# Kernel tuning notes

Measured on AMD Instinct MI355X. Metric: run time of the kernel, lower is better.

The kernel has to match this reference:

```python
import jax, jax.numpy as jnp
import numpy as np

B, C, CI, H, W = 4, 256, 128, 64, 64  # batch, in_channels, inter_channels, spatial


def setup_inputs() -> dict:
    key = jax.random.key(0)
    ks = jax.random.split(key, 9)
    p = lambda k, shape: jax.random.normal(k, shape, jnp.float32) * 0.05
    return {
        "x": jax.random.normal(ks[0], (B, C, H, W), jnp.float32),
        "g_w": p(ks[1], (CI, C)), "g_b": p(ks[2], (CI,)),
        "theta_w": p(ks[3], (CI, C)), "theta_b": p(ks[4], (CI,)),
        "phi_w": p(ks[5], (CI, C)), "phi_b": p(ks[6], (CI,)),
        "out_w": p(ks[7], (C, CI)), "out_b": p(ks[8], (C,)),
    }


def reference(x, g_w, g_b, theta_w, theta_b, phi_w, phi_b, out_w, out_b):
    n, c, h, w = x.shape
    xf = x.reshape(n, c, h * w)  # (b, C, N)
    # 1x1 convs as channel matmuls
    g_x = jnp.einsum('bcn,oc->bno', xf, g_w) + g_b              # (b, N, CI)
    theta_x = jnp.einsum('bcn,oc->bno', xf, theta_w) + theta_b  # (b, N, CI)
    phi_x = jnp.einsum('bcn,oc->bon', xf, phi_w) + phi_b[:, None]  # (b, CI, N)
    # 'channel' whitening: theta centered over channel axis per position,
    # phi centered over spatial axis per channel (as in source)
    theta_x = theta_x - theta_x.mean(axis=2, keepdims=True)
    phi_x = phi_x - phi_x.mean(axis=2, keepdims=True)
    # no softmax / no scaling in this forward
    pairwise = jnp.einsum('bnc,bcm->bnm', theta_x, phi_x)  # (b, N, N)
    y = jnp.einsum('bnm,bmc->bnc', pairwise, g_x)          # (b, N, CI)
    out = jnp.einsum('bnc,oc->bon', y, out_w) + out_b[:, None]  # (b, C, N)
    return x + out.reshape(n, c, h, w)
```

## Files before the change

### kernel.cpp

```cpp
#include <hip/hip_runtime.h>

constexpr int kB  = 4;
constexpr int kC  = 256;
constexpr int kCI = 128;
constexpr int kN  = 64 * 64;


constexpr int kSplits = 16;
constexpr int kSliceN = kN / kSplits;

typedef __attribute__((ext_vector_type(8))) short bf16x8;
typedef __attribute__((ext_vector_type(4))) float f32x4;

__device__ inline ushort f2b(float f) {
    unsigned u = __float_as_uint(f);
    return (ushort)((u + 0x7FFF + ((u >> 16) & 1)) >> 16);
}
__device__ inline float b2f(ushort u) { return __uint_as_float((unsigned)u << 16); }

constexpr long kOffTwcT  = 0;
constexpr long kOffTbc   = kOffTwcT + kC * kCI;
constexpr long kOffPG    = kOffTbc + kCI;
constexpr long kOffRs    = kOffPG + (long)kB * kC * kN / 2;
constexpr long kOffTpart = kOffRs + kB * kC;
constexpr long kOffT     = kOffTpart + (long)kB * kSplits * kCI * kCI;
constexpr long kOffW2t   = kOffT + kB * kCI * kCI;
constexpr long kOffMt    = kOffW2t + kB * kC * kCI;
constexpr long kOffBeta  = kOffMt + kB * kC * kC;
constexpr long kOffXT    = kOffBeta + kB * kC;

__global__ void __launch_bounds__(256, 4)
xt_kernel(const float* __restrict__ x, ushort* __restrict__ xT) {
    int b = blockIdx.z;
    int n0 = blockIdx.x * 64, c0 = blockIdx.y * 64;
    __shared__ float ft[64][66];
    int t = threadIdx.x;
    const float* xb = x + (long)b * kC * kN;
#pragma unroll
    for (int i = 0; i < 4; i++) {
        int l = t + 256 * i;
        int row = l >> 4, col4 = (l & 15) * 4;
        float4 v = *(const float4*)(xb + (long)(c0 + row) * kN + n0 + col4);
        ft[row][col4 + 0] = v.x; ft[row][col4 + 1] = v.y;
        ft[row][col4 + 2] = v.z; ft[row][col4 + 3] = v.w;
    }
    __syncthreads();
    {
        int n = t >> 2, cs = (t & 3) * 16;
        unsigned w[8];
#pragma unroll
        for (int j = 0; j < 8; j++) {
            ushort lo = f2b(ft[cs + 2 * j][n]);
            ushort hi = f2b(ft[cs + 2 * j + 1][n]);
            w[j] = (unsigned)lo | ((unsigned)hi << 16);
        }
        ushort* dst = xT + ((long)b * kN + n0 + n) * kC + c0 + cs;
        ((uint4*)dst)[0] = make_uint4(w[0], w[1], w[2], w[3]);
        ((uint4*)dst)[1] = make_uint4(w[4], w[5], w[6], w[7]);
    }
}

__global__ void centerw_kernel(const float* __restrict__ theta_w,
                               const float* __restrict__ theta_b,
                               float* __restrict__ twcT, float* __restrict__ tbc) {
    __shared__ float sm[128];
    int t = threadIdx.x;
    if (t < 128) sm[t] = theta_b[t];
    __syncthreads();
    for (int st = 64; st > 0; st >>= 1) {
        if (t < st) sm[t] += sm[t + st];
        __syncthreads();
    }
    float bmean = sm[0] * (1.f / kCI);
    float m = 0.f;
    for (int k = 0; k < kCI; k++) m += theta_w[k * kC + t];
    m *= (1.f / kCI);
    for (int k = 0; k < kCI; k++) twcT[t * kCI + k] = theta_w[k * kC + t] - m;
    if (t < 128) tbc[t] = theta_b[t] - bmean;
}

__global__ void __launch_bounds__(256, 2)
pg_mfma(const float* __restrict__ phi_w, const float* __restrict__ g_w,
        const ushort* __restrict__ xT, ushort* __restrict__ PGh) {
    int b = blockIdx.z;
    int r0 = blockIdx.y * 128, n0 = blockIdx.x * 64;
    const float* wbase = blockIdx.y == 0 ? phi_w : g_w;
    __shared__ ushort Ws[128 * 40];
    __shared__ ushort Xs[64 * 40];
    int t = threadIdx.x;
    int w = t >> 6, lane = t & 63, q = lane >> 4, ln = lane & 15;
    f32x4 acc[2][4];
#pragma unroll
    for (int i = 0; i < 2; i++)
#pragma unroll
        for (int j = 0; j < 4; j++) acc[i][j] = 0.f;
    const ushort* xTb = xT + ((long)b * kN + n0) * kC;
    for (int kc = 0; kc < kC; kc += 32) {
        __syncthreads();
#pragma unroll
        for (int it = 0; it < 4; it++) {
            int l = t + 256 * it;
            int row = l >> 3, seg = l & 7;
            float4 v = *(const float4*)(wbase + (long)row * kC + kc + seg * 4);
            ushort4 u = {f2b(v.x), f2b(v.y), f2b(v.z), f2b(v.w)};
            *(ushort4*)&Ws[row * 40 + seg * 4] = u;
        }
        {
            int row = t >> 2, seg = t & 3;
            uint4 v = *(const uint4*)(xTb + (long)row * kC + kc + seg * 8);
            *(uint4*)&Xs[row * 40 + seg * 8] = v;
        }
        __syncthreads();
        bf16x8 a[2], bb[4];
#pragma unroll
        for (int mt = 0; mt < 2; mt++)
            a[mt] = *(const bf16x8*)&Ws[(32 * w + 16 * mt + ln) * 40 + q * 8];
#pragma unroll
        for (int nt = 0; nt < 4; nt++)
            bb[nt] = *(const bf16x8*)&Xs[(16 * nt + ln) * 40 + q * 8];
#pragma unroll
        for (int mt = 0; mt < 2; mt++)
#pragma unroll
            for (int nt = 0; nt < 4; nt++)
                acc[mt][nt] = __builtin_amdgcn_mfma_f32_16x16x32_bf16(
                    a[mt], bb[nt], acc[mt][nt], 0, 0, 0);
    }
    ushort* pb = PGh + (long)b * kC * kN;
#pragma unroll
    for (int mt = 0; mt < 2; mt++)
#pragma unroll
        for (int nt = 0; nt < 4; nt++)
#pragma unroll
            for (int i = 0; i < 4; i++) {
                int row = r0 + 32 * w + 16 * mt + 4 * q + i;
                int col = n0 + 16 * nt + ln;
                pb[(long)row * kN + col] = f2b(acc[mt][nt][i]);
            }
}

__global__ void rowsum_kernel(const ushort* __restrict__ PGh, float* __restrict__ rs) {
    int br = blockIdx.x;
    const ushort* p = PGh + (long)br * kN;
    float s = 0.f;
    for (int i = threadIdx.x * 8; i < kN; i += 2048) {
        uint4 v = *(const uint4*)(p + i);
        unsigned ww[4] = {v.x, v.y, v.z, v.w};
#pragma unroll
        for (int j = 0; j < 4; j++) {
            s += __uint_as_float(ww[j] << 16);
            s += __uint_as_float(ww[j] & 0xFFFF0000u);
        }
    }
    __shared__ float sm[256];
    sm[threadIdx.x] = s;
    __syncthreads();
    for (int st = 128; st > 0; st >>= 1) {
        if (threadIdx.x < st) sm[threadIdx.x] += sm[threadIdx.x + st];
        __syncthreads();
    }
    if (threadIdx.x == 0) rs[br] = sm[0];
}

__global__ void __launch_bounds__(256, 4)
tsplit_mfma(const ushort* __restrict__ PGh, float* __restrict__ Tpart) {
    int s = blockIdx.x, b = blockIdx.z;
    int qy = blockIdx.y >> 1, qx = blockIdx.y & 1;
    long nbase = (long)s * kSliceN;
    __shared__ ushort As[64 * 40];
    __shared__ ushort Bs[64 * 40];
    int t = threadIdx.x;
    int w = t >> 6, lane = t & 63, q = lane >> 4, ln = lane & 15;
    f32x4 acc[4];
#pragma unroll
    for (int j = 0; j < 4; j++) acc[j] = 0.f;
    const ushort* Phi = PGh + ((long)b * kC + 64 * qy) * kN + nbase;
    const ushort* G2  = PGh + ((long)b * kC + kCI + 64 * qx) * kN + nbase;
    for (int kc = 0; kc < kSliceN; kc += 32) {
        __syncthreads();
        {
            int row = t >> 2, seg = t & 3;
            *(uint4*)&As[row * 40 + seg * 8] =
                *(const uint4*)(Phi + (long)row * kN + kc + seg * 8);
            *(uint4*)&Bs[row * 40 + seg * 8] =
                *(const uint4*)(G2 + (long)row * kN + kc + seg * 8);
        }
        __syncthreads();
        bf16x8 a = *(const bf16x8*)&As[(16 * w + ln) * 40 + q * 8];
#pragma unroll
        for (int nt = 0; nt < 4; nt++) {
            bf16x8 bb = *(const bf16x8*)&Bs[(16 * nt + ln) * 40 + q * 8];
            acc[nt] = __builtin_amdgcn_mfma_f32_16x16x32_bf16(a, bb, acc[nt], 0, 0, 0);
        }
    }
    float* Tp = Tpart + ((long)b * kSplits + s) * kCI * kCI;
#pragma unroll
    for (int nt = 0; nt < 4; nt++)
#pragma unroll
        for (int i = 0; i < 4; i++) {
            int c  = 64 * qy + 16 * w + 4 * q + i;
            int cp = 64 * qx + 16 * nt + ln;
            Tp[(long)c * kCI + cp] = acc[nt][i];
        }
}

__global__ void treduce_kernel(const float* __restrict__ Tpart, const float* __restrict__ rs,
                               float* __restrict__ T) {
    int idx = blockIdx.x * 256 + threadIdx.x;
    int b = idx >> 14;
    int c = (idx >> 7) & 127, cp = idx & 127;
    const float* tp = Tpart + (long)b * kSplits * kCI * kCI + (idx & 16383);
    float s = 0.f;
#pragma unroll
    for (int sl = 0; sl < kSplits; sl++) s += tp[(long)sl * kCI * kCI];
    s -= rs[b * kC + c] * rs[b * kC + kCI + cp] * (1.f / kN);
    T[idx] = s;
}

__global__ void __launch_bounds__(256, 4)
nt64_gemm(const float* __restrict__ A, const float* __restrict__ B,
          float* __restrict__ Cm, int M, int N, int K,
          long sA, long sB, long sC) {
    int b = blockIdx.z;
    const float* Ab = A + (long)b * sA;
    const float* Bb = B + (long)b * sB;
    float* Cb = Cm + (long)b * sC;
    __shared__ __align__(16) float As[16][68];
    __shared__ __align__(16) float Bs[16][68];
    int t = threadIdx.x;
    int tx = t & 15, ty = t >> 4;
    int m0 = blockIdx.y * 64, n0 = blockIdx.x * 64;
    float acc[4][4] = {};
    for (int kc = 0; kc < K; kc += 16) {
        __syncthreads();
        {
            int r = t >> 2, c4 = (t & 3) * 4;
            float4 va = *(const float4*)(Ab + (long)(m0 + r) * K + kc + c4);
            As[c4 + 0][r] = va.x; As[c4 + 1][r] = va.y;
            As[c4 + 2][r] = va.z; As[c4 + 3][r] = va.w;
            float4 vb = *(const float4*)(Bb + (long)(n0 + r) * K + kc + c4);
            Bs[c4 + 0][r] = vb.x; Bs[c4 + 1][r] = vb.y;
            Bs[c4 + 2][r] = vb.z; Bs[c4 + 3][r] = vb.w;
        }
        __syncthreads();
#pragma unroll
        for (int k = 0; k < 16; k++) {
            float4 a = *(const float4*)&As[k][4 * ty];
            float4 bv = *(const float4*)&Bs[k][4 * tx];
            float av[4] = {a.x, a.y, a.z, a.w};
            float bw[4] = {bv.x, bv.y, bv.z, bv.w};
#pragma unroll
            for (int i = 0; i < 4; i++)
#pragma unroll
                for (int j = 0; j < 4; j++) acc[i][j] += av[i] * bw[j];
        }
    }
#pragma unroll
    for (int i = 0; i < 4; i++) {
        float4 ov = {acc[i][0], acc[i][1], acc[i][2], acc[i][3]};
        *(float4*)(Cb + (long)(m0 + 4 * ty + i) * N + n0 + 4 * tx) = ov;
    }
}

__global__ void beta_kernel(const float* __restrict__ W2t, const float* __restrict__ tbc,
                            const float* __restrict__ out_b, float* __restrict__ beta) {
    int i = blockIdx.x * blockDim.x + threadIdx.x;
    if (i >= kB * kC) return;
    int o = i & (kC - 1);
    float s = out_b[o];
    const float* row = W2t + (long)i * kCI;
#pragma unroll 8
    for (int k = 0; k < kCI; k++) s += tbc[k] * row[k];
    beta[i] = s;
}

__global__ void __launch_bounds__(256, 2)
final_mfma(const float* __restrict__ x, const float* __restrict__ Mt,
           const ushort* __restrict__ xT, const float* __restrict__ beta,
           float* __restrict__ out) {
    int b = blockIdx.z;
    int o0 = blockIdx.y * 128, n0 = blockIdx.x * 64;
    const float* Mb = Mt + (long)b * kC * kC;
    __shared__ ushort Ws[128 * 40];
    __shared__ ushort Xs[64 * 40];
    int t = threadIdx.x;
    int w = t >> 6, lane = t & 63, q = lane >> 4, ln = lane & 15;
    f32x4 acc[2][4];
#pragma unroll
    for (int i = 0; i < 2; i++)
#pragma unroll
        for (int j = 0; j < 4; j++) acc[i][j] = 0.f;
    const ushort* xTb = xT + ((long)b * kN + n0) * kC;
    for (int kc = 0; kc < kC; kc += 32) {
        __syncthreads();
#pragma unroll
        for (int it = 0; it < 4; it++) {
            int l = t + 256 * it;
            int row = l >> 3, seg = l & 7;
            float4 v = *(const float4*)(Mb + (long)(o0 + row) * kC + kc + seg * 4);
            ushort4 u = {f2b(v.x), f2b(v.y), f2b(v.z), f2b(v.w)};
            *(ushort4*)&Ws[row * 40 + seg * 4] = u;
        }
        {
            int row = t >> 2, seg = t & 3;
            uint4 v = *(const uint4*)(xTb + (long)row * kC + kc + seg * 8);
            *(uint4*)&Xs[row * 40 + seg * 8] = v;
        }
        __syncthreads();
        bf16x8 a[2], bb[4];
#pragma unroll
        for (int mt = 0; mt < 2; mt++)
            a[mt] = *(const bf16x8*)&Ws[(32 * w + 16 * mt + ln) * 40 + q * 8];
#pragma unroll
        for (int nt = 0; nt < 4; nt++)
            bb[nt] = *(const bf16x8*)&Xs[(16 * nt + ln) * 40 + q * 8];
#pragma unroll
        for (int mt = 0; mt < 2; mt++)
#pragma unroll
            for (int nt = 0; nt < 4; nt++)
                acc[mt][nt] = __builtin_amdgcn_mfma_f32_16x16x32_bf16(
                    a[mt], bb[nt], acc[mt][nt], 0, 0, 0);
    }
    const float* xb = x + (long)b * kC * kN;
    float* ob = out + (long)b * kC * kN;
#pragma unroll
    for (int mt = 0; mt < 2; mt++)
#pragma unroll
        for (int nt = 0; nt < 4; nt++)
#pragma unroll
            for (int i = 0; i < 4; i++) {
                int row = o0 + 32 * w + 16 * mt + 4 * q + i;
                int col = n0 + 16 * nt + ln;
                long idx = (long)row * kN + col;
                ob[idx] = acc[mt][nt][i] + xb[idx] + beta[b * kC + row];
            }
}

extern "C" void kernel_launch(void* const* d_in, const int* in_sizes, int n_in,
                              void* d_out, int out_size, void* d_ws, size_t ws_size,
                              hipStream_t stream) {
    const float* x       = (const float*)d_in[0];
    const float* g_w     = (const float*)d_in[1];
    const float* theta_w = (const float*)d_in[3];
    const float* theta_b = (const float*)d_in[4];
    const float* phi_w   = (const float*)d_in[5];
    const float* out_w   = (const float*)d_in[7];
    const float* out_b   = (const float*)d_in[8];
    float* out = (float*)d_out;
    float* ws  = (float*)d_ws;

    float*  twcT  = ws + kOffTwcT;
    float*  tbc   = ws + kOffTbc;
    ushort* PGh   = (ushort*)(ws + kOffPG);
    float*  rs    = ws + kOffRs;
    float*  Tpart = ws + kOffTpart;
    float*  T     = ws + kOffT;
    float*  W2t   = ws + kOffW2t;
    float*  Mt    = ws + kOffMt;
    float*  beta  = ws + kOffBeta;
    ushort* xT    = (ushort*)(ws + kOffXT);

    xt_kernel<<<dim3(kN / 64, kC / 64, kB), 256, 0, stream>>>(x, xT);
    centerw_kernel<<<1, 256, 0, stream>>>(theta_w, theta_b, twcT, tbc);
    pg_mfma<<<dim3(kN / 64, 2, kB), 256, 0, stream>>>(phi_w, g_w, xT, PGh);
    rowsum_kernel<<<kB * kC, 256, 0, stream>>>(PGh, rs);
    tsplit_mfma<<<dim3(kSplits, 4, kB), 256, 0, stream>>>(PGh, Tpart);
    treduce_kernel<<<kB * kCI * kCI / 256, 256, 0, stream>>>(Tpart, rs, T);
    nt64_gemm<<<dim3(2, 4, kB), 256, 0, stream>>>(out_w, T, W2t, kC, kCI, kCI,
                                                  0, (long)kCI * kCI, (long)kC * kCI);
    nt64_gemm<<<dim3(4, 4, kB), 256, 0, stream>>>(W2t, twcT, Mt, kC, kC, kCI,
                                                  (long)kC * kCI, 0, (long)kC * kC);
    beta_kernel<<<kB, 256, 0, stream>>>(W2t, tbc, out_b, beta);
    final_mfma<<<dim3(kN / 64, 2, kB), 256, 0, stream>>>(x, Mt, xT, beta, out);
}
```

Measured before the change: 151.0 us.

## Fuse rowsum into pg_mfma, beta into Mt GEMM, parallelize centering, use bf16 residual

Row sums of the phi/g projections are now accumulated in the pg_mfma epilogue with wave shuffles and atomics, replacing the separate rowsum pass over PGh. The centering kernel is split across four blocks with a shared-memory tile, and it also zeroes the row-sum buffer. The beta bias vector is computed inside a new Mt GEMM kernel, removing the separate beta launch. The final kernel reads the residual from the bf16 transposed copy of x instead of the fp32 input, cutting that traffic at the cost of residual precision and less coalesced reads.

```diff
diff --git a/kernel.cpp b/kernel.cpp
--- a/kernel.cpp
+++ b/kernel.cpp
@@ -60,28 +60,60 @@
     }
 }
 
-__global__ void centerw_kernel(const float* __restrict__ theta_w,
-                               const float* __restrict__ theta_b,
-                               float* __restrict__ twcT, float* __restrict__ tbc) {
+__global__ void __launch_bounds__(256, 2)
+centerw_kernel(const float* __restrict__ theta_w, const float* __restrict__ theta_b,
+               float* __restrict__ twcT, float* __restrict__ tbc,
+               float* __restrict__ rs) {
+    int blk = blockIdx.x;
+    int c0 = blk * 64;
+    int t = threadIdx.x;
+    __shared__ float Ls[128][65];
+    __shared__ float part[64][4];
+    __shared__ float mean[64];
     __shared__ float sm[128];
-    int t = threadIdx.x;
-    if (t < 128) sm[t] = theta_b[t];
+    rs[blk * 256 + t] = 0.f;
+#pragma unroll
+    for (int it = 0; it < 8; it++) {
+        int l = t + 256 * it;
+        int k = l >> 4, c4 = (l & 15) * 4;
+        float4 v = *(const float4*)(theta_w + (long)k * kC + c0 + c4);
+        Ls[k][c4 + 0] = v.x; Ls[k][c4 + 1] = v.y;
+        Ls[k][c4 + 2] = v.z; Ls[k][c4 + 3] = v.w;
+    }
     __syncthreads();
-    for (int st = 64; st > 0; st >>= 1) {
-        if (t < st) sm[t] += sm[t + st];
-        __syncthreads();
-    }
-    float bmean = sm[0] * (1.f / kCI);
-    float m = 0.f;
-    for (int k = 0; k < kCI; k++) m += theta_w[k * kC + t];
-    m *= (1.f / kCI);
-    for (int k = 0; k < kCI; k++) twcT[t * kCI + k] = theta_w[k * kC + t] - m;
-    if (t < 128) tbc[t] = theta_b[t] - bmean;
+    {
+        int c = t >> 2, q = t & 3;
+        float s = 0.f;
+#pragma unroll
+        for (int k = 0; k < 32; k++) s += Ls[q * 32 + k][c];
+        part[c][q] = s;
+    }
+    __syncthreads();
+    if (t < 64) mean[t] = (part[t][0] + part[t][1] + part[t][2] + part[t][3]) * (1.f / kCI);
+    __syncthreads();
+    {
+        int c = t >> 2, ks = (t & 3) * 32;
+        float* dst = twcT + (long)(c0 + c) * kCI + ks;
+        float m = mean[c];
+#pragma unroll
+        for (int k = 0; k < 32; k++) dst[k] = Ls[ks + k][c] - m;
+    }
+    if (blk == 0) {
+        if (t < 128) sm[t] = theta_b[t];
+        __syncthreads();
+        for (int st = 64; st > 0; st >>= 1) {
+            if (t < st) sm[t] += sm[t + st];
+            __syncthreads();
+        }
+        float bmean = sm[0] * (1.f / kCI);
+        if (t < 128) tbc[t] = theta_b[t] - bmean;
+    }
 }
 
 __global__ void __launch_bounds__(256, 2)
 pg_mfma(const float* __restrict__ phi_w, const float* __restrict__ g_w,
-        const ushort* __restrict__ xT, ushort* __restrict__ PGh) {
+        const ushort* __restrict__ xT, ushort* __restrict__ PGh,
+        float* __restrict__ rs) {
     int b = blockIdx.z;
     int r0 = blockIdx.y * 128, n0 = blockIdx.x * 64;
     const float* wbase = blockIdx.y == 0 ? phi_w : g_w;
@@ -126,6 +158,7 @@
                     a[mt], bb[nt], acc[mt][nt], 0, 0, 0);
     }
     ushort* pb = PGh + (long)b * kC * kN;
+    float rpart[2][4] = {};
 #pragma unroll
     for (int mt = 0; mt < 2; mt++)
 #pragma unroll
@@ -134,31 +167,22 @@
             for (int i = 0; i < 4; i++) {
                 int row = r0 + 32 * w + 16 * mt + 4 * q + i;
                 int col = n0 + 16 * nt + ln;
-                pb[(long)row * kN + col] = f2b(acc[mt][nt][i]);
+                ushort st = f2b(acc[mt][nt][i]);
+                pb[(long)row * kN + col] = st;
+                rpart[mt][i] += b2f(st);
             }
-}
-
-__global__ void rowsum_kernel(const ushort* __restrict__ PGh, float* __restrict__ rs) {
-    int br = blockIdx.x;
-    const ushort* p = PGh + (long)br * kN;
-    float s = 0.f;
-    for (int i = threadIdx.x * 8; i < kN; i += 2048) {
-        uint4 v = *(const uint4*)(p + i);
-        unsigned ww[4] = {v.x, v.y, v.z, v.w};
-#pragma unroll
-        for (int j = 0; j < 4; j++) {
-            s += __uint_as_float(ww[j] << 16);
-            s += __uint_as_float(ww[j] & 0xFFFF0000u);
-        }
-    }
-    __shared__ float sm[256];
-    sm[threadIdx.x] = s;
-    __syncthreads();
-    for (int st = 128; st > 0; st >>= 1) {
-        if (threadIdx.x < st) sm[threadIdx.x] += sm[threadIdx.x + st];
-        __syncthreads();
-    }
-    if (threadIdx.x == 0) rs[br] = sm[0];
+#pragma unroll
+    for (int mt = 0; mt < 2; mt++)
+#pragma unroll
+        for (int i = 0; i < 4; i++) {
+            float v = rpart[mt][i];
+            v += __shfl_xor(v, 1);
+            v += __shfl_xor(v, 2);
+            v += __shfl_xor(v, 4);
+            v += __shfl_xor(v, 8);
+            if (ln == 0)
+                atomicAdd(rs + b * kC + r0 + 32 * w + 16 * mt + 4 * q + i, v);
+        }
 }
 
 __global__ void __launch_bounds__(256, 4)
@@ -261,22 +285,62 @@
     }
 }
 
-__global__ void beta_kernel(const float* __restrict__ W2t, const float* __restrict__ tbc,
-                            const float* __restrict__ out_b, float* __restrict__ beta) {
-    int i = blockIdx.x * blockDim.x + threadIdx.x;
-    if (i >= kB * kC) return;
-    int o = i & (kC - 1);
-    float s = out_b[o];
-    const float* row = W2t + (long)i * kCI;
-#pragma unroll 8
-    for (int k = 0; k < kCI; k++) s += tbc[k] * row[k];
-    beta[i] = s;
+__global__ void __launch_bounds__(256, 4)
+mt_gemm(const float* __restrict__ W2t, const float* __restrict__ twcT,
+        const float* __restrict__ tbc, const float* __restrict__ out_b,
+        float* __restrict__ Mt, float* __restrict__ betaOut) {
+    int b = blockIdx.z;
+    const float* Ab = W2t + (long)b * kC * kCI;
+    float* Cb = Mt + (long)b * kC * kC;
+    __shared__ __align__(16) float As[16][68];
+    __shared__ __align__(16) float Bs[16][68];
+    __shared__ float tbcS[kCI];
+    int t = threadIdx.x;
+    int tx = t & 15, ty = t >> 4;
+    int m0 = blockIdx.y * 64, n0 = blockIdx.x * 64;
+    if (t < kCI) tbcS[t] = tbc[t];
+    float acc[4][4] = {};
+    float bacc = 0.f;
+    for (int kc = 0; kc < kCI; kc += 16) {
+        __syncthreads();
+        {
+            int r = t >> 2, c4 = (t & 3) * 4;
+            float4 va = *(const float4*)(Ab + (long)(m0 + r) * kCI + kc + c4);
+            As[c4 + 0][r] = va.x; As[c4 + 1][r] = va.y;
+            As[c4 + 2][r] = va.z; As[c4 + 3][r] = va.w;
+            float4 vb = *(const float4*)(twcT + (long)(n0 + r) * kCI + kc + c4);
+            Bs[c4 + 0][r] = vb.x; Bs[c4 + 1][r] = vb.y;
+            Bs[c4 + 2][r] = vb.z; Bs[c4 + 3][r] = vb.w;
+        }
+        __syncthreads();
+#pragma unroll
+        for (int k = 0; k < 16; k++) {
+            float4 a = *(const float4*)&As[k][4 * ty];
+            float4 bv = *(const float4*)&Bs[k][4 * tx];
+            float av[4] = {a.x, a.y, a.z, a.w};
+            float bw[4] = {bv.x, bv.y, bv.z, bv.w};
+#pragma unroll
+            for (int i = 0; i < 4; i++)
+#pragma unroll
+                for (int j = 0; j < 4; j++) acc[i][j] += av[i] * bw[j];
+        }
+        if (blockIdx.x == 0 && t < 64) {
+#pragma unroll
+            for (int c = 0; c < 16; c++) bacc += tbcS[kc + c] * As[c][t];
+        }
+    }
+#pragma unroll
+    for (int i = 0; i < 4; i++) {
+        float4 ov = {acc[i][0], acc[i][1], acc[i][2], acc[i][3]};
+        *(float4*)(Cb + (long)(m0 + 4 * ty + i) * kC + n0 + 4 * tx) = ov;
+    }
+    if (blockIdx.x == 0 && t < 64)
+        betaOut[b * kC + m0 + t] = bacc + out_b[m0 + t];
 }
 
 __global__ void __launch_bounds__(256, 2)
-final_mfma(const float* __restrict__ x, const float* __restrict__ Mt,
-           const ushort* __restrict__ xT, const float* __restrict__ beta,
-           float* __restrict__ out) {
+final_mfma(const float* __restrict__ Mt, const ushort* __restrict__ xT,
+           const float* __restrict__ beta, float* __restrict__ out) {
     int b = blockIdx.z;
     int o0 = blockIdx.y * 128, n0 = blockIdx.x * 64;
     const float* Mb = Mt + (long)b * kC * kC;
@@ -320,19 +384,23 @@
                 acc[mt][nt] = __builtin_amdgcn_mfma_f32_16x16x32_bf16(
                     a[mt], bb[nt], acc[mt][nt], 0, 0, 0);
     }
-    const float* xb = x + (long)b * kC * kN;
+    const ushort* xTr = xT + (long)b * kN * kC;
     float* ob = out + (long)b * kC * kN;
 #pragma unroll
     for (int mt = 0; mt < 2; mt++)
 #pragma unroll
-        for (int nt = 0; nt < 4; nt++)
+        for (int nt = 0; nt < 4; nt++) {
+            int col = n0 + 16 * nt + ln;
+            int rowb = o0 + 32 * w + 16 * mt + 4 * q;
+            uint2 rv = *(const uint2*)(xTr + (long)col * kC + rowb);
+            ushort r4[4] = {(ushort)(rv.x & 0xFFFF), (ushort)(rv.x >> 16),
+                            (ushort)(rv.y & 0xFFFF), (ushort)(rv.y >> 16)};
 #pragma unroll
             for (int i = 0; i < 4; i++) {
-                int row = o0 + 32 * w + 16 * mt + 4 * q + i;
-                int col = n0 + 16 * nt + ln;
-                long idx = (long)row * kN + col;
-                ob[idx] = acc[mt][nt][i] + xb[idx] + beta[b * kC + row];
+                int row = rowb + i;
+                ob[(long)row * kN + col] = acc[mt][nt][i] + b2f(r4[i]) + beta[b * kC + row];
             }
+        }
 }
 
 extern "C" void kernel_launch(void* const* d_in, const int* in_sizes, int n_in,
@@ -360,15 +428,12 @@
     ushort* xT    = (ushort*)(ws + kOffXT);
 
     xt_kernel<<<dim3(kN / 64, kC / 64, kB), 256, 0, stream>>>(x, xT);
-    centerw_kernel<<<1, 256, 0, stream>>>(theta_w, theta_b, twcT, tbc);
-    pg_mfma<<<dim3(kN / 64, 2, kB), 256, 0, stream>>>(phi_w, g_w, xT, PGh);
-    rowsum_kernel<<<kB * kC, 256, 0, stream>>>(PGh, rs);
+    centerw_kernel<<<4, 256, 0, stream>>>(theta_w, theta_b, twcT, tbc, rs);
+    pg_mfma<<<dim3(kN / 64, 2, kB), 256, 0, stream>>>(phi_w, g_w, xT, PGh, rs);
     tsplit_mfma<<<dim3(kSplits, 4, kB), 256, 0, stream>>>(PGh, Tpart);
     treduce_kernel<<<kB * kCI * kCI / 256, 256, 0, stream>>>(Tpart, rs, T);
     nt64_gemm<<<dim3(2, 4, kB), 256, 0, stream>>>(out_w, T, W2t, kC, kCI, kCI,
                                                   0, (long)kCI * kCI, (long)kC * kCI);
-    nt64_gemm<<<dim3(4, 4, kB), 256, 0, stream>>>(W2t, twcT, Mt, kC, kC, kCI,
-                                                  (long)kC * kCI, 0, (long)kC * kC);
-    beta_kernel<<<kB, 256, 0, stream>>>(W2t, tbc, out_b, beta);
-    final_mfma<<<dim3(kN / 64, 2, kB), 256, 0, stream>>>(x, Mt, xT, beta, out);
-}
+    mt_gemm<<<dim3(4, 4, kB), 256, 0, stream>>>(W2t, twcT, tbc, out_b, Mt, beta);
+    final_mfma<<<dim3(kN / 64, 2, kB), 256, 0, stream>>>(Mt, xT, beta, out);
+}
```

Result: slower. 168.3 us (+11.5%).
